# Kernel optimization log

Hardware: AMD Instinct MI355X
Metric: run time of the kernel (lower is better)

The kernel has to match this reference:

```python
import jax, jax.numpy as jnp
import numpy as np

NUM_HEADS = 16
LN_EPS = 1e-5


def setup_inputs() -> dict:
    key = jax.random.key(0)
    ks = jax.random.split(key, 5)
    B, S, H = 32768, 3, 1024
    scale = 1.0 / np.sqrt(H)
    return {
        "slots": jax.random.normal(ks[0], (B, S, H), dtype=jnp.float32),
        "in_proj_w": jax.random.normal(ks[1], (3 * H, H), dtype=jnp.float32) * scale,
        "in_proj_b": jax.random.normal(ks[2], (3 * H,), dtype=jnp.float32) * 0.02,
        "out_w": jax.random.normal(ks[3], (H, H), dtype=jnp.float32) * scale,
        "out_b": jax.random.normal(ks[4], (H,), dtype=jnp.float32) * 0.02,
        "ln_g": jnp.ones((H,), dtype=jnp.float32),
        "ln_b": jnp.zeros((H,), dtype=jnp.float32),
    }


def reference(slots, in_proj_w, in_proj_b, out_w, out_b, ln_g, ln_b):
    # slots: [B, 3, H]. Matches torch nn.MultiheadAttention (batch_first) in eval
    # mode (dropout inactive) followed by residual add + LayerNorm.
    B, S, H = slots.shape
    nh = NUM_HEADS
    dh = H // nh

    # fused QKV projection: torch does x @ in_proj_w.T + in_proj_b
    qkv = jnp.einsum("bsh,eh->bse", slots, in_proj_w) + in_proj_b  # [B,S,3H]
    q, k, v = jnp.split(qkv, 3, axis=-1)

    def heads(t):  # [B,S,H] -> [B,nh,S,dh]
        return t.reshape(B, S, nh, dh).transpose(0, 2, 1, 3)

    q, k, v = heads(q), heads(k), heads(v)

    scores = jnp.einsum("bnqd,bnkd->bnqk", q, k) / jnp.sqrt(jnp.asarray(dh, slots.dtype))
    attn = jax.nn.softmax(scores, axis=-1)  # [B,nh,3,3]
    ctx = jnp.einsum("bnqk,bnkd->bnqd", attn, v)  # [B,nh,3,dh]
    ctx = ctx.transpose(0, 2, 1, 3).reshape(B, S, H)

    attn_out = jnp.einsum("bsh,oh->bso", ctx, out_w) + out_b  # out_proj

    # residual + LayerNorm (dropout is identity at inference)
    y = slots + attn_out
    mu = jnp.mean(y, axis=-1, keepdims=True)
    var = jnp.mean(jnp.square(y - mu), axis=-1, keepdims=True)
    return (y - mu) / jnp.sqrt(var + LN_EPS) * ln_g + ln_b
```

## Files before the change

kernel.cpp:

```cpp
#include <hip/hip_runtime.h>
#include <stdint.h>

typedef unsigned short u16;
typedef float f32x4 __attribute__((ext_vector_type(4)));
typedef short bf16x8 __attribute__((ext_vector_type(8)));

__device__ __forceinline__ u16 f2bu(float f) {
  uint32_t x = __builtin_bit_cast(uint32_t, f);
  x += 0x7fffu + ((x >> 16) & 1u);
  return (u16)(x >> 16);
}
__device__ __forceinline__ float b2f(u16 u) {
  return __builtin_bit_cast(float, (uint32_t)u << 16);
}
__device__ __forceinline__ void gll16(const void* g, void* l) {
  __builtin_amdgcn_global_load_lds(
      (const __attribute__((address_space(1))) void*)g,
      (__attribute__((address_space(3))) void*)l, 16, 0, 0);
}

__global__ __launch_bounds__(256) void cvt_all_kernel(
    const float* __restrict__ s, u16* __restrict__ os, int ns4,
    const float* __restrict__ w1, u16* __restrict__ o1, int n14,
    const float* __restrict__ w2, u16* __restrict__ o2, int n24) {
  const int stride = gridDim.x * 256;
  const int t0 = blockIdx.x * 256 + threadIdx.x;
  for (int i = t0; i < ns4; i += stride) {
    f32x4 f = __builtin_nontemporal_load(&reinterpret_cast<const f32x4*>(s)[i]);
    ushort4 o;
    o.x = f2bu(f.x); o.y = f2bu(f.y); o.z = f2bu(f.z); o.w = f2bu(f.w);
    reinterpret_cast<ushort4*>(os)[i] = o;
  }
  for (int i = t0; i < n14; i += stride) {
    f32x4 f = __builtin_nontemporal_load(&reinterpret_cast<const f32x4*>(w1)[i]);
    ushort4 o;
    o.x = f2bu(f.x); o.y = f2bu(f.y); o.z = f2bu(f.z); o.w = f2bu(f.w);
    reinterpret_cast<ushort4*>(o1)[i] = o;
  }
  for (int i = t0; i < n24; i += stride) {
    f32x4 f = __builtin_nontemporal_load(&reinterpret_cast<const f32x4*>(w2)[i]);
    ushort4 o;
    o.x = f2bu(f.x); o.y = f2bu(f.y); o.z = f2bu(f.z); o.w = f2bu(f.w);
    reinterpret_cast<ushort4*>(o2)[i] = o;
  }
}

__global__ __launch_bounds__(1024, 4) void gemm256_bt_bias(
    const u16* __restrict__ A, const u16* __restrict__ Bw,
    const float* __restrict__ bias, u16* __restrict__ C,
    int N, int K, int lda, int ldc, int ntn) {
  __shared__ u16 lds[2][2][16384];
  const int tid = threadIdx.x;
  const int lane = tid & 63, wid = tid >> 6;
  const int wr = wid >> 2, wc = wid & 3;
  const int fr = lane & 15, kg = lane >> 4;

  const int cpx = (int)gridDim.x >> 3;
  const int bid = blockIdx.x;
  const int sid = (bid & 7) * cpx + (bid >> 3);
  const int mt = sid / ntn, nt = sid % ntn;

  const int srow = tid >> 3;
  const int sc8 = (tid & 7) ^ (srow & 7);
  const u16* Ag = A + (size_t)(mt * 256 + srow) * lda + sc8 * 8;
  const u16* Bg = Bw + (size_t)(nt * 256 + srow) * K + sc8 * 8;
  const size_t arstep = (size_t)128 * lda;
  const size_t brstep = (size_t)128 * K;

  const int fx = fr & 7;
  const int aoff = (wr * 64 + fr) * 64;
  const int boff = (wc * 64 + fr) * 64;

  f32x4 acc[4][4];
#pragma unroll
  for (int i = 0; i < 4; i++)
#pragma unroll
    for (int j = 0; j < 4; j++) acc[i][j] = f32x4{0.f, 0.f, 0.f, 0.f};

  const int NT = K >> 6;

#define STAGE(b, kt) do {                                                  \
    const u16* a_ = Ag + (size_t)(kt) * 64;                                \
    const u16* b_ = Bg + (size_t)(kt) * 64;                                \
    gll16(a_,          &lds[(b)][0][wid * 512]);                           \
    gll16(a_ + arstep, &lds[(b)][0][8192 + wid * 512]);                    \
    gll16(b_,          &lds[(b)][1][wid * 512]);                           \
    gll16(b_ + brstep, &lds[(b)][1][8192 + wid * 512]);                    \
  } while (0)

  STAGE(0, 0);
  __syncthreads();

  for (int t = 0; t < NT; t++) {
    const int cur = t & 1;
    if (t + 1 < NT) STAGE(cur ^ 1, t + 1);
    const u16* As = &lds[cur][0][0];
    const u16* Bs = &lds[cur][1][0];
#pragma unroll
    for (int kh = 0; kh < 2; kh++) {
      const int slot3 = ((kh << 2) | kg) ^ fx;
      bf16x8 a[4], b[4];
#pragma unroll
      for (int nj = 0; nj < 4; nj++)
        b[nj] = *(const bf16x8*)&Bs[boff + nj * 1024 + slot3 * 8];
#pragma unroll
      for (int mi = 0; mi < 4; mi++)
        a[mi] = *(const bf16x8*)&As[aoff + mi * 1024 + slot3 * 8];
      __builtin_amdgcn_s_setprio(1);
#pragma unroll
      for (int mi = 0; mi < 4; mi++)
#pragma unroll
        for (int nj = 0; nj < 4; nj++)
          acc[mi][nj] = __builtin_amdgcn_mfma_f32_16x16x32_bf16(
              a[mi], b[nj], acc[mi][nj], 0, 0, 0);
      __builtin_amdgcn_s_setprio(0);
    }
    __syncthreads();
  }
#undef STAGE

  const int crow0 = mt * 256 + wr * 64 + kg * 4;
  const int ccol0 = nt * 256 + wc * 64 + fr;
#pragma unroll
  for (int nj = 0; nj < 4; nj++) {
    const int col = ccol0 + nj * 16;
    const float bb = bias[col];
#pragma unroll
    for (int mi = 0; mi < 4; mi++) {
      const int r0 = crow0 + mi * 16;
      f32x4 v = acc[mi][nj];
#pragma unroll
      for (int r = 0; r < 4; r++)
        C[(size_t)(r0 + r) * ldc + col] = f2bu(v[r] + bb);
    }
  }
}

__global__ __launch_bounds__(256) void attn3_kernel(
    u16* __restrict__ qkv) {
  const int tid = threadIdx.x;
  const int lane = tid & 63, wid = tid >> 6;
  const int nunit = 32768 * 2;
  for (int unit = blockIdx.x * 4 + wid; unit < nunit; unit += gridDim.x * 4) {
    const int b = unit >> 1, hf = unit & 1;
    const int colb = hf * 512 + (lane >> 3) * 64 + (lane & 7) * 8;
    const size_t base = (size_t)b * 9216 + colb;

    float q[3][8], k[3][8], v[3][8];
#pragma unroll
    for (int s = 0; s < 3; s++) {
      bf16x8 uq = __builtin_nontemporal_load(
          (const bf16x8*)(qkv + base + (size_t)s * 3072));
      bf16x8 uk = __builtin_nontemporal_load(
          (const bf16x8*)(qkv + base + (size_t)s * 3072 + 1024));
      bf16x8 uv = __builtin_nontemporal_load(
          (const bf16x8*)(qkv + base + (size_t)s * 3072 + 2048));
#pragma unroll
      for (int e = 0; e < 8; e++) {
        q[s][e] = b2f((u16)uq[e]);
        k[s][e] = b2f((u16)uk[e]);
        v[s][e] = b2f((u16)uv[e]);
      }
    }

    float sc[3][3];
#pragma unroll
    for (int i = 0; i < 3; i++)
#pragma unroll
      for (int j = 0; j < 3; j++) {
        float p = 0.f;
#pragma unroll
        for (int e = 0; e < 8; e++) p += q[i][e] * k[j][e];
        p += __shfl_xor(p, 1);
        p += __shfl_xor(p, 2);
        p += __shfl_xor(p, 4);
        sc[i][j] = p;
      }

    float o[3][8];
#pragma unroll
    for (int i = 0; i < 3; i++) {
      float mx = fmaxf(sc[i][0], fmaxf(sc[i][1], sc[i][2]));
      float e0 = __expf((sc[i][0] - mx) * 0.125f);
      float e1 = __expf((sc[i][1] - mx) * 0.125f);
      float e2 = __expf((sc[i][2] - mx) * 0.125f);
      float inv = 1.f / (e0 + e1 + e2);
      e0 *= inv; e1 *= inv; e2 *= inv;
#pragma unroll
      for (int e = 0; e < 8; e++)
        o[i][e] = e0 * v[0][e] + e1 * v[1][e] + e2 * v[2][e];
    }

#pragma unroll
    for (int i = 0; i < 3; i++) {
      bf16x8 ov;
#pragma unroll
      for (int e = 0; e < 8; e++) ov[e] = (short)f2bu(o[i][e]);
      *(bf16x8*)(qkv + base + (size_t)i * 3072 + 1024) = ov;
    }
  }
}

__global__ __launch_bounds__(256) void ln_kernel(
    const u16* __restrict__ slots_bf, const u16* __restrict__ ao,
    const float* __restrict__ g, const float* __restrict__ bvec,
    float* __restrict__ out) {
  const int tid = threadIdx.x;
  const int lane = tid & 63, wid = tid >> 6;
  const int row = blockIdx.x * 4 + wid;
  const size_t rb = (size_t)row * 1024;
  const size_t ab = (size_t)row * 3072;

  float y[16];
  float sum = 0.f, sq = 0.f;
#pragma unroll
  for (int c = 0; c < 2; c++) {
    const int col = c * 512 + lane * 8;
    bf16x8 s8 = __builtin_nontemporal_load((const bf16x8*)(slots_bf + rb + col));
    bf16x8 a8 = __builtin_nontemporal_load((const bf16x8*)(ao + ab + col));
#pragma unroll
    for (int e = 0; e < 8; e++) {
      float yv = b2f((u16)s8[e]) + b2f((u16)a8[e]);
      y[c * 8 + e] = yv;
      sum += yv;
      sq += yv * yv;
    }
  }
#pragma unroll
  for (int m = 1; m < 64; m <<= 1) {
    sum += __shfl_xor(sum, m);
    sq  += __shfl_xor(sq, m);
  }
  const float mu = sum * (1.0f / 1024.0f);
  const float var = sq * (1.0f / 1024.0f) - mu * mu;
  const float rs = rsqrtf(var + 1e-5f);
#pragma unroll
  for (int c = 0; c < 2; c++) {
    const int col = c * 512 + lane * 8;
#pragma unroll
    for (int h = 0; h < 2; h++) {
      const float* gp = g + col + h * 4;
      const float* bp = bvec + col + h * 4;
      f32x4 gg = *reinterpret_cast<const f32x4*>(gp);
      f32x4 bb = *reinterpret_cast<const f32x4*>(bp);
      f32x4 ov;
      ov.x = (y[c * 8 + h * 4 + 0] - mu) * rs * gg.x + bb.x;
      ov.y = (y[c * 8 + h * 4 + 1] - mu) * rs * gg.y + bb.y;
      ov.z = (y[c * 8 + h * 4 + 2] - mu) * rs * gg.z + bb.z;
      ov.w = (y[c * 8 + h * 4 + 3] - mu) * rs * gg.w + bb.w;
      __builtin_nontemporal_store(ov, reinterpret_cast<f32x4*>(out + rb + col + h * 4));
    }
  }
}

extern "C" void kernel_launch(void* const* d_in, const int* in_sizes, int n_in,
                              void* d_out, int out_size, void* d_ws, size_t ws_size,
                              hipStream_t stream) {
  const float* slots = (const float*)d_in[0];
  const float* in_w  = (const float*)d_in[1];
  const float* in_b  = (const float*)d_in[2];
  const float* out_w = (const float*)d_in[3];
  const float* out_b = (const float*)d_in[4];
  const float* ln_g  = (const float*)d_in[5];
  const float* ln_b  = (const float*)d_in[6];
  float* out = (float*)d_out;

  const int M = 32768 * 3;

  char* ws = (char*)d_ws;
  u16* Abf   = (u16*)ws;
  u16* Winb  = (u16*)(ws + 201326592);
  u16* Woutb = (u16*)(ws + 207618048);
  u16* qkv   = (u16*)(ws + 209715200);

  cvt_all_kernel<<<2048, 256, 0, stream>>>(
      slots, Abf, M * 1024 / 4,
      in_w, Winb, 3072 * 1024 / 4,
      out_w, Woutb, 1024 * 1024 / 4);

  gemm256_bt_bias<<<384 * 12, 1024, 0, stream>>>(
      Abf, Winb, in_b, qkv, 3072, 1024, 1024, 3072, 12);

  attn3_kernel<<<2048, 256, 0, stream>>>(qkv);

  gemm256_bt_bias<<<384 * 4, 1024, 0, stream>>>(
      qkv + 1024, Woutb, out_b, qkv, 1024, 1024, 3072, 3072, 4);

  ln_kernel<<<M / 4, 256, 0, stream>>>(Abf, qkv, ln_g, ln_b, out);
}
```

Measured before the change: 1.303 ms.

## Triple-buffer GEMM LDS with K=32 stages and vmcnt-based waits

Restructures the bf16 GEMM main loop from a double-buffered 64-wide K tile to a triple-buffered 32-wide K tile, prefetching two stages ahead. It uses explicit s_waitcnt vmcnt plus a raw barrier in place of __syncthreads, so loads for later stages can stay in flight across the barrier. The LDS swizzle is redone for the new 32-element row layout. This aims to hide global-to-LDS latency better, at the cost of twice as many barriers per K and less MFMA work per barrier.

```diff
diff --git a/kernel.cpp b/kernel.cpp
--- a/kernel.cpp
+++ b/kernel.cpp
@@ -4,6 +4,8 @@
 typedef unsigned short u16;
 typedef float f32x4 __attribute__((ext_vector_type(4)));
 typedef short bf16x8 __attribute__((ext_vector_type(8)));
+
+#define MEMFENCE asm volatile("" ::: "memory")
 
 __device__ __forceinline__ u16 f2bu(float f) {
   uint32_t x = __builtin_bit_cast(uint32_t, f);
@@ -49,7 +51,7 @@
     const u16* __restrict__ A, const u16* __restrict__ Bw,
     const float* __restrict__ bias, u16* __restrict__ C,
     int N, int K, int lda, int ldc, int ntn) {
-  __shared__ u16 lds[2][2][16384];
+  __shared__ u16 lds[3][2][8192];
   const int tid = threadIdx.x;
   const int lane = tid & 63, wid = tid >> 6;
   const int wr = wid >> 2, wc = wid & 3;
@@ -60,16 +62,15 @@
   const int sid = (bid & 7) * cpx + (bid >> 3);
   const int mt = sid / ntn, nt = sid % ntn;
 
-  const int srow = tid >> 3;
-  const int sc8 = (tid & 7) ^ (srow & 7);
-  const u16* Ag = A + (size_t)(mt * 256 + srow) * lda + sc8 * 8;
-  const u16* Bg = Bw + (size_t)(nt * 256 + srow) * K + sc8 * 8;
-  const size_t arstep = (size_t)128 * lda;
-  const size_t brstep = (size_t)128 * K;
-
-  const int fx = fr & 7;
-  const int aoff = (wr * 64 + fr) * 64;
-  const int boff = (wc * 64 + fr) * 64;
+  const int srow = tid >> 2;
+  const int scol = (tid & 3) ^ ((tid >> 3) & 3);
+  const u16* Ag = A + (size_t)(mt * 256 + srow) * lda + scol * 8;
+  const u16* Bg = Bw + (size_t)(nt * 256 + srow) * K + scol * 8;
+
+  const int sw = (fr >> 1) & 3;
+  const int kgs = (kg ^ sw) * 8;
+  const int aoff = (wr * 64 + fr) * 32 + kgs;
+  const int boff = (wc * 64 + fr) * 32 + kgs;
 
   f32x4 acc[4][4];
 #pragma unroll
@@ -77,45 +78,45 @@
 #pragma unroll
     for (int j = 0; j < 4; j++) acc[i][j] = f32x4{0.f, 0.f, 0.f, 0.f};
 
-  const int NT = K >> 6;
-
-#define STAGE(b, kt) do {                                                  \
-    const u16* a_ = Ag + (size_t)(kt) * 64;                                \
-    const u16* b_ = Bg + (size_t)(kt) * 64;                                \
-    gll16(a_,          &lds[(b)][0][wid * 512]);                           \
-    gll16(a_ + arstep, &lds[(b)][0][8192 + wid * 512]);                    \
-    gll16(b_,          &lds[(b)][1][wid * 512]);                           \
-    gll16(b_ + brstep, &lds[(b)][1][8192 + wid * 512]);                    \
+  const int NT = K >> 5;
+
+#define STAGE(b, kt) do {                                   \
+    gll16(Ag + (size_t)(kt) * 32, &lds[(b)][0][wid * 512]); \
+    gll16(Bg + (size_t)(kt) * 32, &lds[(b)][1][wid * 512]); \
   } while (0)
 
   STAGE(0, 0);
-  __syncthreads();
-
+  STAGE(1, 1);
+  asm volatile("s_waitcnt vmcnt(2)" ::: "memory");
+  __builtin_amdgcn_s_barrier();
+  MEMFENCE;
+
+  int cur = 0, stg = 2;
   for (int t = 0; t < NT; t++) {
-    const int cur = t & 1;
-    if (t + 1 < NT) STAGE(cur ^ 1, t + 1);
+    if (t + 2 < NT) STAGE(stg, t + 2);
     const u16* As = &lds[cur][0][0];
     const u16* Bs = &lds[cur][1][0];
-#pragma unroll
-    for (int kh = 0; kh < 2; kh++) {
-      const int slot3 = ((kh << 2) | kg) ^ fx;
-      bf16x8 a[4], b[4];
+    bf16x8 a[4], b[4];
+#pragma unroll
+    for (int nj = 0; nj < 4; nj++)
+      b[nj] = *(const bf16x8*)&Bs[boff + nj * 512];
+#pragma unroll
+    for (int mi = 0; mi < 4; mi++)
+      a[mi] = *(const bf16x8*)&As[aoff + mi * 512];
+    __builtin_amdgcn_s_setprio(1);
+#pragma unroll
+    for (int mi = 0; mi < 4; mi++)
 #pragma unroll
       for (int nj = 0; nj < 4; nj++)
-        b[nj] = *(const bf16x8*)&Bs[boff + nj * 1024 + slot3 * 8];
-#pragma unroll
-      for (int mi = 0; mi < 4; mi++)
-        a[mi] = *(const bf16x8*)&As[aoff + mi * 1024 + slot3 * 8];
-      __builtin_amdgcn_s_setprio(1);
-#pragma unroll
-      for (int mi = 0; mi < 4; mi++)
-#pragma unroll
-        for (int nj = 0; nj < 4; nj++)
-          acc[mi][nj] = __builtin_amdgcn_mfma_f32_16x16x32_bf16(
-              a[mi], b[nj], acc[mi][nj], 0, 0, 0);
-      __builtin_amdgcn_s_setprio(0);
-    }
-    __syncthreads();
+        acc[mi][nj] = __builtin_amdgcn_mfma_f32_16x16x32_bf16(
+            a[mi], b[nj], acc[mi][nj], 0, 0, 0);
+    __builtin_amdgcn_s_setprio(0);
+    if (t < NT - 2)      asm volatile("s_waitcnt vmcnt(2)" ::: "memory");
+    else                 asm volatile("s_waitcnt vmcnt(0)" ::: "memory");
+    __builtin_amdgcn_s_barrier();
+    MEMFENCE;
+    cur = (cur == 2) ? 0 : cur + 1;
+    stg = (stg == 2) ? 0 : stg + 1;
   }
 #undef STAGE
 
```

New measurement: 1.330 ms. 2.1% more time.
